# Kernel tuning notes

Hardware: AMD Instinct MI355X
Metric: run time of the kernel (lower is better)

Reference implementation:

```python
import jax, jax.numpy as jnp
import numpy as np

B, T, C = 2, 2048, 768
H = 12
HD = C // H  # 64
DFF = 4 * C
EPS = 1e-5


def setup_inputs() -> dict:
    key = jax.random.key(0)
    ks = jax.random.split(key, 12)
    s = 0.02
    return {
        "x": jax.random.normal(ks[0], (B, T, C), dtype=jnp.float32),
        "ln1_g": jnp.ones((C,), jnp.float32),
        "ln1_b": jnp.zeros((C,), jnp.float32),
        "w_qkv": jax.random.normal(ks[1], (C, 3 * C), dtype=jnp.float32) * s,
        "w_o": jax.random.normal(ks[2], (C, C), dtype=jnp.float32) * s,
        "ln2_g": jnp.ones((C,), jnp.float32),
        "ln2_b": jnp.zeros((C,), jnp.float32),
        "w_fc": jax.random.normal(ks[3], (C, DFF), dtype=jnp.float32) * s,
        "b_fc": jnp.zeros((DFF,), jnp.float32),
        "w_proj": jax.random.normal(ks[4], (DFF, C), dtype=jnp.float32) * s,
        "b_proj": jnp.zeros((C,), jnp.float32),
    }


def _layernorm(x, g, b):
    mu = jnp.mean(x, axis=-1, keepdims=True)
    var = jnp.mean(jnp.square(x - mu), axis=-1, keepdims=True)
    return (x - mu) * jax.lax.rsqrt(var + EPS) * g + b


def _attn(x, w_qkv, w_o):
    b, t, c = x.shape
    qkv = x @ w_qkv  # [b,t,3c]
    q, k, v = jnp.split(qkv, 3, axis=-1)
    q = q.reshape(b, t, H, HD).transpose(0, 2, 1, 3)  # [b,h,t,d]
    k = k.reshape(b, t, H, HD).transpose(0, 2, 1, 3)
    v = v.reshape(b, t, H, HD).transpose(0, 2, 1, 3)
    att = jnp.einsum("bhqd,bhkd->bhqk", q, k) / jnp.sqrt(jnp.float32(HD))
    causal = jnp.tril(jnp.ones((t, t), dtype=bool))
    att = jnp.where(causal, att, -jnp.inf)
    att = jax.nn.softmax(att, axis=-1)
    y = jnp.einsum("bhqk,bhkd->bhqd", att, v)
    y = y.transpose(0, 2, 1, 3).reshape(b, t, c)
    return y @ w_o


def reference(x, ln1_g, ln1_b, w_qkv, w_o, ln2_g, ln2_b, w_fc, b_fc, w_proj, b_proj):
    x = x + _attn(_layernorm(x, ln1_g, ln1_b), w_qkv, w_o)
    h = _layernorm(x, ln2_g, ln2_b)
    h = jax.nn.gelu(h @ w_fc + b_fc, approximate=False)  # torch F.gelu default = exact erf
    x = x + (h @ w_proj + b_proj)
    return x
```

## Files before the change

kernel.cpp:

```cpp
#include <hip/hip_runtime.h>
#include <hip/hip_bf16.h>
#include <math.h>

#define T_SEQ 2048
#define NB 2
#define C_DIM 768
#define NH 12

typedef unsigned short ushort_t;
typedef __attribute__((ext_vector_type(8))) short short8;
typedef __attribute__((ext_vector_type(8))) unsigned short ushort8;
typedef __attribute__((ext_vector_type(4))) unsigned short ushortx4;
typedef __attribute__((ext_vector_type(4))) float floatx4;
typedef __attribute__((ext_vector_type(4))) _Float16 half4;

__device__ inline float bf2f(ushort_t u) {
    unsigned int x = ((unsigned int)u) << 16;
    return __uint_as_float(x);
}
__device__ inline ushort_t f2bf(float f) {
    unsigned int u = __float_as_uint(f);
    unsigned int r = (u + 0x7fffu + ((u >> 16) & 1u)) >> 16;
    return (ushort_t)r;
}
__device__ inline ushort_t f2h_bits(float f) {
    union { _Float16 h; ushort_t u; } cv;
    cv.h = (_Float16)f;
    return cv.u;
}

#if defined(__has_builtin)
#if __has_builtin(__builtin_amdgcn_global_load_lds)
#define HAVE_GLL 1
#endif
#endif

__device__ inline void gload_lds16(const ushort_t* g, ushort_t* l) {
#ifdef HAVE_GLL
    __builtin_amdgcn_global_load_lds(
        (const __attribute__((address_space(1))) void*)g,
        (__attribute__((address_space(3))) void*)l, 16, 0, 0);
#else
    int lane = threadIdx.x & 63;
    *(ushort8*)(l + lane * 8) = *(const ushort8*)g;
#endif
}

__global__ __launch_bounds__(256) void ln_kernel(const float* __restrict__ x,
                                                 const float* __restrict__ g,
                                                 const float* __restrict__ b,
                                                 ushort_t* __restrict__ out) {
    int row = blockIdx.x;
    int tid = threadIdx.x;
    int lane = tid & 63, wave = tid >> 6;
    const float* xr = x + (size_t)row * C_DIM;
    float v0 = xr[tid];
    float v1 = xr[tid + 256];
    float v2 = xr[tid + 512];
    float s = v0 + v1 + v2;
#pragma unroll
    for (int m = 32; m > 0; m >>= 1) s += __shfl_xor(s, m, 64);
    __shared__ float red[8];
    if (lane == 0) red[wave] = s;
    __syncthreads();
    float mean = (red[0] + red[1] + red[2] + red[3]) * (1.0f / C_DIM);
    float d0 = v0 - mean, d1 = v1 - mean, d2 = v2 - mean;
    float q = d0 * d0 + d1 * d1 + d2 * d2;
#pragma unroll
    for (int m = 32; m > 0; m >>= 1) q += __shfl_xor(q, m, 64);
    if (lane == 0) red[wave + 4] = q;
    __syncthreads();
    float var = (red[4] + red[5] + red[6] + red[7]) * (1.0f / C_DIM);
    float rstd = rsqrtf(var + 1e-5f);
    ushort_t* orow = out + (size_t)row * C_DIM;
    orow[tid]       = f2bf(d0 * rstd * g[tid]       + b[tid]);
    orow[tid + 256] = f2bf(d1 * rstd * g[tid + 256] + b[tid + 256]);
    orow[tid + 512] = f2bf(d2 * rstd * g[tid + 512] + b[tid + 512]);
}

__global__ __launch_bounds__(192) void combine_ln_kernel(const float* __restrict__ x,
                                                         const ushort_t* __restrict__ P,
                                                         const float* __restrict__ g,
                                                         const float* __restrict__ bb,
                                                         float* __restrict__ x2,
                                                         ushort_t* __restrict__ xn) {
    int row = blockIdx.x;
    int tid = threadIdx.x;
    int lane = tid & 63, wave = tid >> 6;
    int col = tid * 4;
    size_t idx = (size_t)row * C_DIM + col;
    floatx4 xv = *(const floatx4*)&x[idx];
    ushortx4 a = *(const ushortx4*)&P[idx];
    ushortx4 b2 = *(const ushortx4*)&P[3145728 + idx];
    floatx4 v;
#pragma unroll
    for (int j = 0; j < 4; j++) v[j] = xv[j] + bf2f(a[j]) + bf2f(b2[j]);
    *(floatx4*)&x2[idx] = v;

    float s = v[0] + v[1] + v[2] + v[3];
#pragma unroll
    for (int m = 32; m > 0; m >>= 1) s += __shfl_xor(s, m, 64);
    __shared__ float red[6];
    if (lane == 0) red[wave] = s;
    __syncthreads();
    float mean = (red[0] + red[1] + red[2]) * (1.0f / C_DIM);
    floatx4 d;
#pragma unroll
    for (int j = 0; j < 4; j++) d[j] = v[j] - mean;
    float q = d[0] * d[0] + d[1] * d[1] + d[2] * d[2] + d[3] * d[3];
#pragma unroll
    for (int m = 32; m > 0; m >>= 1) q += __shfl_xor(q, m, 64);
    if (lane == 0) red[wave + 3] = q;
    __syncthreads();
    float var = (red[3] + red[4] + red[5]) * (1.0f / C_DIM);
    float rstd = rsqrtf(var + 1e-5f);
    floatx4 gv = *(const floatx4*)&g[col];
    floatx4 bv = *(const floatx4*)&bb[col];
    ushortx4 o;
#pragma unroll
    for (int j = 0; j < 4; j++) o[j] = f2bf(d[j] * rstd * gv[j] + bv[j]);
    *(ushortx4*)&xn[idx] = o;
}

__global__ __launch_bounds__(256) void wconv_kernel(const float* __restrict__ W,
                                                    ushort_t* __restrict__ WT,
                                                    int K, int N) {
    __shared__ ushort_t Tls[64 * 72];
    int tid = threadIdx.x;
    int k0 = blockIdx.x * 64, n0 = blockIdx.y * 64;
    int nl = (tid & 15) * 4;
    int kl = tid >> 4;
#pragma unroll
    for (int rr = 0; rr < 4; rr++) {
        int k = kl + rr * 16;
        floatx4 v = *(const floatx4*)&W[(size_t)(k0 + k) * N + n0 + nl];
#pragma unroll
        for (int j = 0; j < 4; j++) Tls[(nl + j) * 72 + k] = f2bf(v[j]);
    }
    __syncthreads();
    int no = tid >> 3;
    int ko = (tid & 7) * 8;
#pragma unroll
    for (int rr = 0; rr < 2; rr++) {
        int n = no + rr * 32;
        ushort8 t = *(const ushort8*)&Tls[n * 72 + ko];
        *(ushort8*)&WT[(size_t)(n0 + n) * K + k0 + ko] = t;
    }
}

__global__ __launch_bounds__(256) void kvprep_kernel(const ushort_t* __restrict__ qkv,
                                                     ushort_t* __restrict__ kh,
                                                     ushort_t* __restrict__ vtb) {
    __shared__ ushort_t Tls[64 * 18];
    int tid = threadIdx.x;
    int tb = blockIdx.x, h = blockIdx.y, b = blockIdx.z;
    const ushort_t* src = qkv + (size_t)b * T_SEQ * 2304;
    size_t hb = (size_t)(b * NH + h) * (T_SEQ * 64);

#pragma unroll
    for (int i = 0; i < 4; i++) {
        int idx = tid + i * 256;
        int t = tb * 16 + (idx >> 6), d = idx & 63;
        kh[hb + (size_t)t * 64 + d] = src[(size_t)t * 2304 + 768 + h * 64 + d];
    }
#pragma unroll
    for (int i = 0; i < 4; i++) {
        int idx = tid + i * 256;
        int t = idx >> 6, d = idx & 63;
        Tls[d * 18 + t] = f2h_bits(bf2f(src[(size_t)(tb * 16 + t) * 2304 + 1536 + h * 64 + d]));
    }
    __syncthreads();
    ushort_t* dst = vtb + hb + (size_t)tb * 1024;
#pragma unroll
    for (int i = 0; i < 4; i++) {
        int j = tid + i * 256;
        dst[j] = Tls[(j >> 4) * 18 + (j & 15)];
    }
}

template <int EPI>
__global__ __launch_bounds__(256) void gemm_bt_kernel(const ushort_t* __restrict__ A,
                                                      const ushort_t* __restrict__ BT,
                                                      const float* __restrict__ bias,
                                                      ushort_t* __restrict__ Cout,
                                                      int M, int N, int K) {
    __shared__ ushort_t As[128 * 32];
    __shared__ ushort_t Bs[128 * 32];
    int tid = threadIdx.x;
    int lane = tid & 63, wave = tid >> 6;
    int lane15 = lane & 15, quad = lane >> 4;
    int wr = wave >> 1, wc = wave & 1;
    int row0 = blockIdx.x * 128, col0 = blockIdx.y * 128;

    int sub_row = lane >> 2;
    int sub_k = (lane & 3) * 8;
    const ushort_t* agp0 = A + (size_t)(row0 + wave * 32 + sub_row) * K + sub_k;
    const ushort_t* agp1 = agp0 + (size_t)16 * K;
    const ushort_t* bgp0 = BT + (size_t)(col0 + wave * 32 + sub_row) * K + sub_k;
    const ushort_t* bgp1 = bgp0 + (size_t)16 * K;
    ushort_t* lA0 = &As[wave * 1024];
    ushort_t* lA1 = lA0 + 512;
    ushort_t* lB0 = &Bs[wave * 1024];
    ushort_t* lB1 = lB0 + 512;

    floatx4 acc[4][4];
    floatx4 zero = {0.f, 0.f, 0.f, 0.f};
#pragma unroll
    for (int mt = 0; mt < 4; mt++)
#pragma unroll
        for (int nt = 0; nt < 4; nt++) acc[mt][nt] = zero;

    for (int k0 = 0; k0 < K; k0 += 32) {
        gload_lds16(agp0 + k0, lA0);
        gload_lds16(agp1 + k0, lA1);
        gload_lds16(bgp0 + k0, lB0);
        gload_lds16(bgp1 + k0, lB1);
        __syncthreads();
        short8 af[4], bfm[4];
#pragma unroll
        for (int mt = 0; mt < 4; mt++)
            af[mt] = *(const short8*)&As[(wr * 64 + mt * 16 + lane15) * 32 + quad * 8];
#pragma unroll
        for (int nt = 0; nt < 4; nt++)
            bfm[nt] = *(const short8*)&Bs[(wc * 64 + nt * 16 + lane15) * 32 + quad * 8];
#pragma unroll
        for (int mt = 0; mt < 4; mt++)
#pragma unroll
            for (int nt = 0; nt < 4; nt++)
                acc[mt][nt] = __builtin_amdgcn_mfma_f32_16x16x32_bf16(af[mt], bfm[nt], acc[mt][nt], 0, 0, 0);
        __syncthreads();
    }

#pragma unroll
    for (int mt = 0; mt < 4; mt++) {
        int r_base = row0 + wr * 64 + mt * 16 + quad * 4;
#pragma unroll
        for (int nt = 0; nt < 4; nt++) {
            int cc = col0 + wc * 64 + nt * 16 + lane15;
            float bvv = (EPI == 2) ? bias[cc] : 0.f;
#pragma unroll
            for (int r = 0; r < 4; r++) {
                int rr = r_base + r;
                float v = acc[mt][nt][r] + bvv;
                if (EPI == 2) v = 0.5f * v * (1.f + erff(v * 0.70710678118f));
                Cout[(size_t)rr * N + cc] = f2bf(v);
            }
        }
    }
}

__global__ __launch_bounds__(256) void gemm_bt_split_kernel(const ushort_t* __restrict__ A,
                                                            const ushort_t* __restrict__ BT,
                                                            ushort_t* __restrict__ P,
                                                            int M, int N, int K, int klen) {
    __shared__ ushort_t As[128 * 32];
    __shared__ ushort_t Bs[128 * 32];
    int tid = threadIdx.x;
    int lane = tid & 63, wave = tid >> 6;
    int lane15 = lane & 15, quad = lane >> 4;
    int wr = wave >> 1, wc = wave & 1;
    int row0 = blockIdx.x * 128, col0 = blockIdx.y * 128;
    int kz = blockIdx.z * klen;

    int sub_row = lane >> 2;
    int sub_k = (lane & 3) * 8;
    const ushort_t* agp0 = A + (size_t)(row0 + wave * 32 + sub_row) * K + kz + sub_k;
    const ushort_t* agp1 = agp0 + (size_t)16 * K;
    const ushort_t* bgp0 = BT + (size_t)(col0 + wave * 32 + sub_row) * K + kz + sub_k;
    const ushort_t* bgp1 = bgp0 + (size_t)16 * K;
    ushort_t* lA0 = &As[wave * 1024];
    ushort_t* lA1 = lA0 + 512;
    ushort_t* lB0 = &Bs[wave * 1024];
    ushort_t* lB1 = lB0 + 512;

    floatx4 acc[4][4];
    floatx4 zero = {0.f, 0.f, 0.f, 0.f};
#pragma unroll
    for (int mt = 0; mt < 4; mt++)
#pragma unroll
        for (int nt = 0; nt < 4; nt++) acc[mt][nt] = zero;

    for (int k0 = 0; k0 < klen; k0 += 32) {
        gload_lds16(agp0 + k0, lA0);
        gload_lds16(agp1 + k0, lA1);
        gload_lds16(bgp0 + k0, lB0);
        gload_lds16(bgp1 + k0, lB1);
        __syncthreads();
        short8 af[4], bfm[4];
#pragma unroll
        for (int mt = 0; mt < 4; mt++)
            af[mt] = *(const short8*)&As[(wr * 64 + mt * 16 + lane15) * 32 + quad * 8];
#pragma unroll
        for (int nt = 0; nt < 4; nt++)
            bfm[nt] = *(const short8*)&Bs[(wc * 64 + nt * 16 + lane15) * 32 + quad * 8];
#pragma unroll
        for (int mt = 0; mt < 4; mt++)
#pragma unroll
            for (int nt = 0; nt < 4; nt++)
                acc[mt][nt] = __builtin_amdgcn_mfma_f32_16x16x32_bf16(af[mt], bfm[nt], acc[mt][nt], 0, 0, 0);
        __syncthreads();
    }

    ushort_t* Pz = P + (size_t)blockIdx.z * M * N;
#pragma unroll
    for (int mt = 0; mt < 4; mt++) {
        int r_base = row0 + wr * 64 + mt * 16 + quad * 4;
#pragma unroll
        for (int nt = 0; nt < 4; nt++) {
            int cc = col0 + wc * 64 + nt * 16 + lane15;
#pragma unroll
            for (int r = 0; r < 4; r++)
                Pz[(size_t)(r_base + r) * N + cc] = f2bf(acc[mt][nt][r]);
        }
    }
}

__global__ __launch_bounds__(256) void combine_bias_res_kernel(float* __restrict__ x2,
                                                               const float* __restrict__ bias,
                                                               const ushort_t* __restrict__ P) {
    int i = blockIdx.x * 256 + threadIdx.x;
    int col = (i * 4) % C_DIM;
    floatx4 xv = *(const floatx4*)&x2[i * 4];
    floatx4 bv = *(const floatx4*)&bias[col];
    ushortx4 a = *(const ushortx4*)&P[i * 4];
    ushortx4 b = *(const ushortx4*)&P[3145728 + i * 4];
    floatx4 o;
#pragma unroll
    for (int j = 0; j < 4; j++) o[j] = xv[j] + bv[j] + bf2f(a[j]) + bf2f(b[j]);
    *(floatx4*)&x2[i * 4] = o;
}

#define QSCALE 0.18033688f
__global__ __launch_bounds__(256) void attn_kernel(const ushort_t* __restrict__ qkv,
                                                   const ushort_t* __restrict__ kh,
                                                   const _Float16* __restrict__ vtb,
                                                   ushort_t* __restrict__ y) {
    __shared__ ushort_t Kb[2][4096];
    __shared__ ushort_t Vb[2][4096];
    int tid = threadIdx.x;
    int lane = tid & 63, wave = tid >> 6;
    int lane15 = lane & 15, quad = lane >> 4;
    int qt = 31 - (int)blockIdx.x;
    int q0 = qt * 64;
    int h = blockIdx.y, b = blockIdx.z;
    const ushort_t* base = qkv + (size_t)b * T_SEQ * 2304;
    size_t hb = (size_t)(b * NH + h) * (T_SEQ * 64);
    const ushort_t* khb = kh + hb;
    const ushort_t* vtbb = (const ushort_t*)(vtb + hb);

    int q = q0 + wave * 16 + lane15;
    int qmax_wave = q0 + wave * 16 + 15;
    short8 qf[2];
#pragma unroll
    for (int c = 0; c < 2; c++) {
        ushort8 qv = *(const ushort8*)(base + (size_t)q * 2304 + h * 64 + c * 32 + quad * 8);
        short8 qs;
#pragma unroll
        for (int j = 0; j < 8; j++) qs[j] = (short)f2bf(bf2f(qv[j]) * QSCALE);
        qf[c] = qs;
    }

    floatx4 o[4];
    floatx4 zero = {0.f, 0.f, 0.f, 0.f};
#pragma unroll
    for (int nt = 0; nt < 4; nt++) o[nt] = zero;
    float m_i = -1e30f, l_i = 0.f;

    int tiles = qt + 1;

    {
        int kb = 0;
        if (wave < 2) {
#pragma unroll
            for (int j = 0; j < 4; j++) {
                int r = wave * 4 + j;
                int i = r * 64 + lane;
                int key = i >> 3;
                int seg = ((i & 7) - (key & 7) + 8) & 7;
                gload_lds16(khb + (size_t)(kb + key) * 64 + seg * 8, &Kb[0][(size_t)r * 512]);
            }
        } else {
#pragma unroll
            for (int j = 0; j < 4; j++) {
                int r = (wave - 2) * 4 + j;
                gload_lds16(vtbb + (size_t)(kb >> 4) * 1024 + (size_t)r * 512 + lane * 8,
                            &Vb[0][(size_t)r * 512]);
            }
        }
    }

    for (int t = 0; t < tiles; t++) {
        int kb = t * 64;
        int cur = t & 1;
        __syncthreads();
        if (t + 1 < tiles) {
            int kb2 = kb + 64;
            int nxt = cur ^ 1;
            if (wave < 2) {
#pragma unroll
                for (int j = 0; j < 4; j++) {
                    int r = wave * 4 + j;
                    int i = r * 64 + lane;
                    int key = i >> 3;
                    int seg = ((i & 7) - (key & 7) + 8) & 7;
                    gload_lds16(khb + (size_t)(kb2 + key) * 64 + seg * 8, &Kb[nxt][(size_t)r * 512]);
                }
            } else {
#pragma unroll
                for (int j = 0; j < 4; j++) {
                    int r = (wave - 2) * 4 + j;
                    gload_lds16(vtbb + (size_t)(kb2 >> 4) * 1024 + (size_t)r * 512 + lane * 8,
                                &Vb[nxt][(size_t)r * 512]);
                }
            }
        }

        if (kb <= qmax_wave) {
            const ushort_t* Kc = Kb[cur];
            const _Float16* Vc = (const _Float16*)Vb[cur];

            floatx4 s[4];
#pragma unroll
            for (int sb = 0; sb < 4; sb++) {
                int key = sb * 16 + lane15;
                int s0i = key * 8 + ((quad + key) & 7);
                int s1i = key * 8 + ((quad + 4 + key) & 7);
                short8 kf0 = *(const short8*)(Kc + (size_t)s0i * 8);
                short8 kf1 = *(const short8*)(Kc + (size_t)s1i * 8);
                floatx4 sv = zero;
                sv = __builtin_amdgcn_mfma_f32_16x16x32_bf16(kf0, qf[0], sv, 0, 0, 0);
                sv = __builtin_amdgcn_mfma_f32_16x16x32_bf16(kf1, qf[1], sv, 0, 0, 0);
                s[sb] = sv;
            }

            float sv[4][4];
#pragma unroll
            for (int sb = 0; sb < 4; sb++)
#pragma unroll
                for (int r = 0; r < 4; r++) sv[sb][r] = s[sb][r];
            if (kb + 64 > qmax_wave) {
#pragma unroll
                for (int sb = 0; sb < 4; sb++)
#pragma unroll
                    for (int r = 0; r < 4; r++) {
                        int key = kb + sb * 16 + quad * 4 + r;
                        if (key > q) sv[sb][r] = -INFINITY;
                    }
            }

            float mx = -1e30f;
#pragma unroll
            for (int sb = 0; sb < 4; sb++)
#pragma unroll
                for (int r = 0; r < 4; r++) mx = fmaxf(mx, sv[sb][r]);
            mx = fmaxf(mx, __shfl_xor(mx, 16, 64));
            mx = fmaxf(mx, __shfl_xor(mx, 32, 64));
            float m_new = fmaxf(m_i, mx);
            float alpha = __builtin_amdgcn_exp2f(m_i - m_new);
            float p[4][4];
            float ls = 0.f;
#pragma unroll
            for (int sb = 0; sb < 4; sb++)
#pragma unroll
                for (int r = 0; r < 4; r++) {
                    p[sb][r] = __builtin_amdgcn_exp2f(sv[sb][r] - m_new);
                    ls += p[sb][r];
                }
            ls += __shfl_xor(ls, 16, 64);
            ls += __shfl_xor(ls, 32, 64);
            l_i = l_i * alpha + ls;
            m_i = m_new;
#pragma unroll
            for (int nt = 0; nt < 4; nt++) o[nt] *= alpha;

            half4 pf[4];
#pragma unroll
            for (int sb = 0; sb < 4; sb++)
#pragma unroll
                for (int r = 0; r < 4; r++) pf[sb][r] = (_Float16)p[sb][r];

#pragma unroll
            for (int sb = 0; sb < 4; sb++) {
                const _Float16* vb2 = Vc + (size_t)sb * 1024 + lane15 * 16 + quad * 4;
#pragma unroll
                for (int nt = 0; nt < 4; nt++) {
                    half4 vf = *(const half4*)(vb2 + nt * 256);
                    o[nt] = __builtin_amdgcn_mfma_f32_16x16x16f16(vf, pf[sb], o[nt], 0, 0, 0);
                }
            }
        }
    }

    __syncthreads();
    float* Cm = (float*)Kb;
    float* Co = (float*)Vb;
    if (quad == 0) { Cm[wave * 16 + lane15] = m_i; Cm[64 + wave * 16 + lane15] = l_i; }
#pragma unroll
    for (int nt = 0; nt < 4; nt++)
#pragma unroll
        for (int r = 0; r < 4; r++)
            Co[wave * 1024 + (nt * 16 + quad * 4 + r) * 16 + lane15] = o[nt][r];
    __syncthreads();

    float m0 = Cm[lane15], m1 = Cm[16 + lane15], m2 = Cm[32 + lane15], m3 = Cm[48 + lane15];
    float mg = fmaxf(fmaxf(m0, m1), fmaxf(m2, m3));
    float s0 = __builtin_amdgcn_exp2f(m0 - mg);
    float s1 = __builtin_amdgcn_exp2f(m1 - mg);
    float s2 = __builtin_amdgcn_exp2f(m2 - mg);
    float s3 = __builtin_amdgcn_exp2f(m3 - mg);
    float lg = Cm[64 + lane15] * s0 + Cm[80 + lane15] * s1 + Cm[96 + lane15] * s2 + Cm[112 + lane15] * s3;
    float rcp = 1.f / lg;

    (void)mg; (void)rcp; (void)s0; (void)s1; (void)s2; (void)s3; (void)lg;

    float rcp_w = 1.f / l_i;
    ushort_t* yb = y + (size_t)b * T_SEQ * 768;
#pragma unroll
    for (int nt = 0; nt < 4; nt++) {
        ushortx4 st;
#pragma unroll
        for (int r = 0; r < 4; r++) st[r] = f2bf(o[nt][r] * rcp_w);
        *(ushortx4*)&yb[(size_t)q * 768 + h * 64 + nt * 16 + quad * 4] = st;
    }
}

extern "C" void kernel_launch(void* const* d_in, const int* in_sizes, int n_in,
                              void* d_out, int out_size, void* d_ws, size_t ws_size,
                              hipStream_t stream) {
    (void)in_sizes; (void)n_in; (void)out_size; (void)ws_size;
    const float* x      = (const float*)d_in[0];
    const float* ln1_g  = (const float*)d_in[1];
    const float* ln1_b  = (const float*)d_in[2];
    const float* w_qkv  = (const float*)d_in[3];
    const float* w_o    = (const float*)d_in[4];
    const float* ln2_g  = (const float*)d_in[5];
    const float* ln2_b  = (const float*)d_in[6];
    const float* w_fc   = (const float*)d_in[7];
    const float* b_fc   = (const float*)d_in[8];
    const float* w_proj = (const float*)d_in[9];
    const float* b_proj = (const float*)d_in[10];

    char* ws = (char*)d_ws;
    ushort_t* qkv    = (ushort_t*)(ws);
    ushort_t* PA     = (ushort_t*)(ws);
    ushort_t* hff    = (ushort_t*)(ws);
    ushort_t* ybuf   = (ushort_t*)(ws + 18874368);
    ushort_t* xn     = (ushort_t*)(ws + 25165824);
    ushort_t* kh     = (ushort_t*)(ws + 25165824);
    ushort_t* PB     = (ushort_t*)(ws + 25165824);
    ushort_t* vtb    = (ushort_t*)(ws + 31457280);
    ushort_t* wqkvT  = (ushort_t*)(ws + 37748736);
    ushort_t* woT    = (ushort_t*)(ws + 37748736);
    ushort_t* wfcT   = (ushort_t*)(ws + 41287680);
    ushort_t* wprojT = (ushort_t*)(ws + 41287680);
    float* x2 = (float*)d_out;

    const int M = NB * T_SEQ;

    wconv_kernel<<<dim3(12, 36), 256, 0, stream>>>(w_qkv, wqkvT, 768, 2304);
    ln_kernel<<<dim3(M), 256, 0, stream>>>(x, ln1_g, ln1_b, xn);
    gemm_bt_kernel<0><<<dim3(32, 18), 256, 0, stream>>>(xn, wqkvT, nullptr, qkv, M, 2304, 768);
    kvprep_kernel<<<dim3(128, 12, 2), 256, 0, stream>>>(qkv, kh, vtb);
    attn_kernel<<<dim3(32, 12, 2), 256, 0, stream>>>(qkv, kh, (const _Float16*)vtb, ybuf);
    wconv_kernel<<<dim3(12, 12), 256, 0, stream>>>(w_o, woT, 768, 768);
    gemm_bt_split_kernel<<<dim3(32, 6, 2), 256, 0, stream>>>(ybuf, woT, PA, M, 768, 768, 384);
    combine_ln_kernel<<<dim3(M), 192, 0, stream>>>(x, PA, ln2_g, ln2_b, x2, xn);
    wconv_kernel<<<dim3(12, 48), 256, 0, stream>>>(w_fc, wfcT, 768, 3072);
    gemm_bt_kernel<2><<<dim3(32, 24), 256, 0, stream>>>(xn, wfcT, b_fc, hff, M, 3072, 768);
    wconv_kernel<<<dim3(48, 12), 256, 0, stream>>>(w_proj, wprojT, 3072, 768);
    gemm_bt_split_kernel<<<dim3(32, 6, 2), 256, 0, stream>>>(hff, wprojT, PB, M, 768, 3072, 1536);
    combine_bias_res_kernel<<<dim3(3072), 256, 0, stream>>>(x2, b_proj, PB);
}
```

Before: 325.3 us.

## Double K-tile to 64 with XOR-swizzled LDS, split-K 3 for out-proj

Both GEMM kernels now stage 64-wide K tiles instead of 32. The LDS layout uses an XOR swizzle on 16-byte segments, intended to halve the number of barriers per K and avoid bank conflicts on the fragment reads. The attention output projection now splits K three ways, and combine_ln sums a third partial buffer. Dead cross-wave combine code at the end of attention is removed. The larger LDS footprint per block may reduce occupancy, and the third partial buffer must fit in the workspace region.

```diff
diff --git a/kernel.cpp b/kernel.cpp
--- a/kernel.cpp
+++ b/kernel.cpp
@@ -92,9 +92,10 @@
     floatx4 xv = *(const floatx4*)&x[idx];
     ushortx4 a = *(const ushortx4*)&P[idx];
     ushortx4 b2 = *(const ushortx4*)&P[3145728 + idx];
+    ushortx4 c2 = *(const ushortx4*)&P[6291456 + idx];
     floatx4 v;
 #pragma unroll
-    for (int j = 0; j < 4; j++) v[j] = xv[j] + bf2f(a[j]) + bf2f(b2[j]);
+    for (int j = 0; j < 4; j++) v[j] = xv[j] + bf2f(a[j]) + bf2f(b2[j]) + bf2f(c2[j]);
     *(floatx4*)&x2[idx] = v;
 
     float s = v[0] + v[1] + v[2] + v[3];
@@ -184,24 +185,28 @@
                                                       const float* __restrict__ bias,
                                                       ushort_t* __restrict__ Cout,
                                                       int M, int N, int K) {
-    __shared__ ushort_t As[128 * 32];
-    __shared__ ushort_t Bs[128 * 32];
+    __shared__ ushort_t As[128 * 64];
+    __shared__ ushort_t Bs[128 * 64];
     int tid = threadIdx.x;
     int lane = tid & 63, wave = tid >> 6;
     int lane15 = lane & 15, quad = lane >> 4;
     int wr = wave >> 1, wc = wave & 1;
     int row0 = blockIdx.x * 128, col0 = blockIdx.y * 128;
 
-    int sub_row = lane >> 2;
-    int sub_k = (lane & 3) * 8;
-    const ushort_t* agp0 = A + (size_t)(row0 + wave * 32 + sub_row) * K + sub_k;
-    const ushort_t* agp1 = agp0 + (size_t)16 * K;
-    const ushort_t* bgp0 = BT + (size_t)(col0 + wave * 32 + sub_row) * K + sub_k;
-    const ushort_t* bgp1 = bgp0 + (size_t)16 * K;
-    ushort_t* lA0 = &As[wave * 1024];
-    ushort_t* lA1 = lA0 + 512;
-    ushort_t* lB0 = &Bs[wave * 1024];
-    ushort_t* lB1 = lB0 + 512;
+    int srow = lane >> 3;
+    int sseg = (lane & 7) ^ srow;
+    const ushort_t* ag[4];
+    const ushort_t* bg[4];
+    ushort_t* la[4];
+    ushort_t* lb[4];
+#pragma unroll
+    for (int j = 0; j < 4; j++) {
+        int r = wave * 32 + j * 8;
+        ag[j] = A + (size_t)(row0 + r + srow) * K + sseg * 8;
+        bg[j] = BT + (size_t)(col0 + r + srow) * K + sseg * 8;
+        la[j] = &As[r * 64];
+        lb[j] = &Bs[r * 64];
+    }
 
     floatx4 acc[4][4];
     floatx4 zero = {0.f, 0.f, 0.f, 0.f};
@@ -210,24 +215,28 @@
 #pragma unroll
         for (int nt = 0; nt < 4; nt++) acc[mt][nt] = zero;
 
-    for (int k0 = 0; k0 < K; k0 += 32) {
-        gload_lds16(agp0 + k0, lA0);
-        gload_lds16(agp1 + k0, lA1);
-        gload_lds16(bgp0 + k0, lB0);
-        gload_lds16(bgp1 + k0, lB1);
+    for (int k0 = 0; k0 < K; k0 += 64) {
+#pragma unroll
+        for (int j = 0; j < 4; j++) gload_lds16(ag[j] + k0, la[j]);
+#pragma unroll
+        for (int j = 0; j < 4; j++) gload_lds16(bg[j] + k0, lb[j]);
         __syncthreads();
-        short8 af[4], bfm[4];
-#pragma unroll
-        for (int mt = 0; mt < 4; mt++)
-            af[mt] = *(const short8*)&As[(wr * 64 + mt * 16 + lane15) * 32 + quad * 8];
-#pragma unroll
-        for (int nt = 0; nt < 4; nt++)
-            bfm[nt] = *(const short8*)&Bs[(wc * 64 + nt * 16 + lane15) * 32 + quad * 8];
-#pragma unroll
-        for (int mt = 0; mt < 4; mt++)
+#pragma unroll
+        for (int ko = 0; ko < 2; ko++) {
+            int slot = (quad + ko * 4) ^ (lane15 & 7);
+            short8 af[4], bfm[4];
+#pragma unroll
+            for (int mt = 0; mt < 4; mt++)
+                af[mt] = *(const short8*)&As[(wr * 64 + mt * 16 + lane15) * 64 + slot * 8];
 #pragma unroll
             for (int nt = 0; nt < 4; nt++)
-                acc[mt][nt] = __builtin_amdgcn_mfma_f32_16x16x32_bf16(af[mt], bfm[nt], acc[mt][nt], 0, 0, 0);
+                bfm[nt] = *(const short8*)&Bs[(wc * 64 + nt * 16 + lane15) * 64 + slot * 8];
+#pragma unroll
+            for (int mt = 0; mt < 4; mt++)
+#pragma unroll
+                for (int nt = 0; nt < 4; nt++)
+                    acc[mt][nt] = __builtin_amdgcn_mfma_f32_16x16x32_bf16(af[mt], bfm[nt], acc[mt][nt], 0, 0, 0);
+        }
         __syncthreads();
     }
 
@@ -253,8 +262,8 @@
                                                             const ushort_t* __restrict__ BT,
                                                             ushort_t* __restrict__ P,
                                                             int M, int N, int K, int klen) {
-    __shared__ ushort_t As[128 * 32];
-    __shared__ ushort_t Bs[128 * 32];
+    __shared__ ushort_t As[128 * 64];
+    __shared__ ushort_t Bs[128 * 64];
     int tid = threadIdx.x;
     int lane = tid & 63, wave = tid >> 6;
     int lane15 = lane & 15, quad = lane >> 4;
@@ -262,16 +271,20 @@
     int row0 = blockIdx.x * 128, col0 = blockIdx.y * 128;
     int kz = blockIdx.z * klen;
 
-    int sub_row = lane >> 2;
-    int sub_k = (lane & 3) * 8;
-    const ushort_t* agp0 = A + (size_t)(row0 + wave * 32 + sub_row) * K + kz + sub_k;
-    const ushort_t* agp1 = agp0 + (size_t)16 * K;
-    const ushort_t* bgp0 = BT + (size_t)(col0 + wave * 32 + sub_row) * K + kz + sub_k;
-    const ushort_t* bgp1 = bgp0 + (size_t)16 * K;
-    ushort_t* lA0 = &As[wave * 1024];
-    ushort_t* lA1 = lA0 + 512;
-    ushort_t* lB0 = &Bs[wave * 1024];
-    ushort_t* lB1 = lB0 + 512;
+    int srow = lane >> 3;
+    int sseg = (lane & 7) ^ srow;
+    const ushort_t* ag[4];
+    const ushort_t* bg[4];
+    ushort_t* la[4];
+    ushort_t* lb[4];
+#pragma unroll
+    for (int j = 0; j < 4; j++) {
+        int r = wave * 32 + j * 8;
+        ag[j] = A + (size_t)(row0 + r + srow) * K + kz + sseg * 8;
+        bg[j] = BT + (size_t)(col0 + r + srow) * K + kz + sseg * 8;
+        la[j] = &As[r * 64];
+        lb[j] = &Bs[r * 64];
+    }
 
     floatx4 acc[4][4];
     floatx4 zero = {0.f, 0.f, 0.f, 0.f};
@@ -280,24 +293,28 @@
 #pragma unroll
         for (int nt = 0; nt < 4; nt++) acc[mt][nt] = zero;
 
-    for (int k0 = 0; k0 < klen; k0 += 32) {
-        gload_lds16(agp0 + k0, lA0);
-        gload_lds16(agp1 + k0, lA1);
-        gload_lds16(bgp0 + k0, lB0);
-        gload_lds16(bgp1 + k0, lB1);
+    for (int k0 = 0; k0 < klen; k0 += 64) {
+#pragma unroll
+        for (int j = 0; j < 4; j++) gload_lds16(ag[j] + k0, la[j]);
+#pragma unroll
+        for (int j = 0; j < 4; j++) gload_lds16(bg[j] + k0, lb[j]);
         __syncthreads();
-        short8 af[4], bfm[4];
-#pragma unroll
-        for (int mt = 0; mt < 4; mt++)
-            af[mt] = *(const short8*)&As[(wr * 64 + mt * 16 + lane15) * 32 + quad * 8];
-#pragma unroll
-        for (int nt = 0; nt < 4; nt++)
-            bfm[nt] = *(const short8*)&Bs[(wc * 64 + nt * 16 + lane15) * 32 + quad * 8];
-#pragma unroll
-        for (int mt = 0; mt < 4; mt++)
+#pragma unroll
+        for (int ko = 0; ko < 2; ko++) {
+            int slot = (quad + ko * 4) ^ (lane15 & 7);
+            short8 af[4], bfm[4];
+#pragma unroll
+            for (int mt = 0; mt < 4; mt++)
+                af[mt] = *(const short8*)&As[(wr * 64 + mt * 16 + lane15) * 64 + slot * 8];
 #pragma unroll
             for (int nt = 0; nt < 4; nt++)
-                acc[mt][nt] = __builtin_amdgcn_mfma_f32_16x16x32_bf16(af[mt], bfm[nt], acc[mt][nt], 0, 0, 0);
+                bfm[nt] = *(const short8*)&Bs[(wc * 64 + nt * 16 + lane15) * 64 + slot * 8];
+#pragma unroll
+            for (int mt = 0; mt < 4; mt++)
+#pragma unroll
+                for (int nt = 0; nt < 4; nt++)
+                    acc[mt][nt] = __builtin_amdgcn_mfma_f32_16x16x32_bf16(af[mt], bfm[nt], acc[mt][nt], 0, 0, 0);
+        }
         __syncthreads();
     }
 
@@ -490,28 +507,6 @@
             }
         }
     }
-
-    __syncthreads();
-    float* Cm = (float*)Kb;
-    float* Co = (float*)Vb;
-    if (quad == 0) { Cm[wave * 16 + lane15] = m_i; Cm[64 + wave * 16 + lane15] = l_i; }
-#pragma unroll
-    for (int nt = 0; nt < 4; nt++)
-#pragma unroll
-        for (int r = 0; r < 4; r++)
-            Co[wave * 1024 + (nt * 16 + quad * 4 + r) * 16 + lane15] = o[nt][r];
-    __syncthreads();
-
-    float m0 = Cm[lane15], m1 = Cm[16 + lane15], m2 = Cm[32 + lane15], m3 = Cm[48 + lane15];
-    float mg = fmaxf(fmaxf(m0, m1), fmaxf(m2, m3));
-    float s0 = __builtin_amdgcn_exp2f(m0 - mg);
-    float s1 = __builtin_amdgcn_exp2f(m1 - mg);
-    float s2 = __builtin_amdgcn_exp2f(m2 - mg);
-    float s3 = __builtin_amdgcn_exp2f(m3 - mg);
-    float lg = Cm[64 + lane15] * s0 + Cm[80 + lane15] * s1 + Cm[96 + lane15] * s2 + Cm[112 + lane15] * s3;
-    float rcp = 1.f / lg;
-
-    (void)mg; (void)rcp; (void)s0; (void)s1; (void)s2; (void)s3; (void)lg;
 
     float rcp_w = 1.f / l_i;
     ushort_t* yb = y + (size_t)b * T_SEQ * 768;
@@ -563,7 +558,7 @@
     kvprep_kernel<<<dim3(128, 12, 2), 256, 0, stream>>>(qkv, kh, vtb);
     attn_kernel<<<dim3(32, 12, 2), 256, 0, stream>>>(qkv, kh, (const _Float16*)vtb, ybuf);
     wconv_kernel<<<dim3(12, 12), 256, 0, stream>>>(w_o, woT, 768, 768);
-    gemm_bt_split_kernel<<<dim3(32, 6, 2), 256, 0, stream>>>(ybuf, woT, PA, M, 768, 768, 384);
+    gemm_bt_split_kernel<<<dim3(32, 6, 3), 256, 0, stream>>>(ybuf, woT, PA, M, 768, 768, 256);
     combine_ln_kernel<<<dim3(M), 192, 0, stream>>>(x, PA, ln2_g, ln2_b, x2, xn);
     wconv_kernel<<<dim3(12, 48), 256, 0, stream>>>(w_fc, wfcT, 768, 3072);
     gemm_bt_kernel<2><<<dim3(32, 24), 256, 0, stream>>>(xn, wfcT, b_fc, hff, M, 3072, 768);
```

Result: faster. 308.4 us (-5.2%).
